# Optimization experiments

Hardware: AMD Instinct MI355X
Metric: run time of the kernel (lower is better)

## Reference

```python
import math
import jax, jax.numpy as jnp
import numpy as np

NUM_HEADS = 16

def _alibi_slopes(n):
    def pow2(n):
        start = 2 ** (-2 ** (-(math.log2(n) - 3)))
        return [start * start ** i for i in range(n)]
    if math.log2(n).is_integer():
        return pow2(n)
    c = 2 ** math.floor(math.log2(n))
    return pow2(c) + _alibi_slopes(2 * c)[0::2][: n - c]

def _alibi_bias(num_heads, L):
    pos = np.arange(L)
    rel = (pos[None, :] - pos[:, None]).astype(np.float32)  # [L, L]
    slopes = np.asarray(_alibi_slopes(num_heads), dtype=np.float32)[:, None, None]
    bias = slopes * rel[None, :, :]  # [H, L, L]
    causal = pos[None, :] <= pos[:, None]
    bias = np.where(causal[None, :, :], bias, -np.inf).astype(np.float32)
    return jnp.asarray(bias)[None]  # [1, H, L, L]

def setup_inputs() -> dict:
    key = jax.random.key(0)
    ks = jax.random.split(key, 4)
    B, L, D = 2, 2048, 1024
    x = jax.random.normal(ks[0], (B, L, D), dtype=jnp.float32)
    W_in = jax.random.normal(ks[1], (D, 3 * D), dtype=jnp.float32) * 0.02
    b_in = jnp.zeros((3 * D,), dtype=jnp.float32)
    W_out = jax.random.normal(ks[2], (D, D), dtype=jnp.float32) * 0.02
    b_out = jnp.zeros((D,), dtype=jnp.float32)
    return {"x": x, "W_in": W_in, "b_in": b_in, "W_out": W_out, "b_out": b_out}

def reference(x, W_in, b_in, W_out, b_out):
    B, L, D = x.shape
    H = NUM_HEADS
    Dh = D // H
    qkv = x @ W_in + b_in  # [B, L, 3D]
    q, k, v = jnp.split(qkv, 3, axis=-1)
    # [B, H, L, Dh]
    q = q.reshape(B, L, H, Dh).transpose(0, 2, 1, 3)
    k = k.reshape(B, L, H, Dh).transpose(0, 2, 1, 3)
    v = v.reshape(B, L, H, Dh).transpose(0, 2, 1, 3)
    attn = jnp.einsum("bhqd,bhkd->bhqk", q, k) * (1.0 / math.sqrt(Dh))
    attn = attn + _alibi_bias(H, L)  # ALiBi + causal mask (-inf above diag)
    p = jax.nn.softmax(attn, axis=-1)
    out = jnp.einsum("bhqk,bhkd->bhqd", p, v)
    out = out.transpose(0, 2, 1, 3).reshape(B, L, D)
    out = out @ W_out + b_out
    return out, k, v
```

## Files before the change

### kernel.cpp

```cpp
#include <hip/hip_runtime.h>
#include <math.h>

typedef __bf16 bf16x8 __attribute__((ext_vector_type(8)));
typedef float  f32x4  __attribute__((ext_vector_type(4)));
typedef unsigned short u16x4 __attribute__((ext_vector_type(4)));

#define BATCH  2
#define SEQ    2048
#define DMODEL 1024
#define NHEAD  16
#define DHEAD  64
#define MROWS  4096
#define N_QKV  3072
#define KDIM   1024
#define OUTSECT (MROWS*DMODEL)

#define LOG2E 1.44269504088896f
#define QSCALE (0.125f * LOG2E)

__device__ inline __bf16 f2bf(float f) {
    unsigned u = __builtin_bit_cast(unsigned, f);
    unsigned r = (u + 0x7fffu + ((u >> 16) & 1u)) >> 16;
    return __builtin_bit_cast(__bf16, (unsigned short)r);
}

__device__ inline void gload16(const void* g, void* l) {
    __builtin_amdgcn_global_load_lds(
        (const __attribute__((address_space(1))) void*)g,
        (__attribute__((address_space(3))) void*)l, 16, 0, 0);
}

__device__ inline float dpp_max16(float x) {
    int v, t;
    v = __builtin_bit_cast(int, x);
    t = __builtin_amdgcn_update_dpp(v, v, 0xB1, 0xF, 0xF, false);
    x = fmaxf(x, __builtin_bit_cast(float, t));
    v = __builtin_bit_cast(int, x);
    t = __builtin_amdgcn_update_dpp(v, v, 0x4E, 0xF, 0xF, false);
    x = fmaxf(x, __builtin_bit_cast(float, t));
    v = __builtin_bit_cast(int, x);
    t = __builtin_amdgcn_update_dpp(v, v, 0x128, 0xF, 0xF, false);
    x = fmaxf(x, __builtin_bit_cast(float, t));
    v = __builtin_bit_cast(int, x);
    t = __builtin_amdgcn_update_dpp(v, v, 0x140, 0xF, 0xF, false);
    x = fmaxf(x, __builtin_bit_cast(float, t));
    return x;
}
__device__ inline float dpp_sum16(float x) {
    int v, t;
    v = __builtin_bit_cast(int, x);
    t = __builtin_amdgcn_update_dpp(v, v, 0xB1, 0xF, 0xF, false);
    x += __builtin_bit_cast(float, t);
    v = __builtin_bit_cast(int, x);
    t = __builtin_amdgcn_update_dpp(v, v, 0x4E, 0xF, 0xF, false);
    x += __builtin_bit_cast(float, t);
    v = __builtin_bit_cast(int, x);
    t = __builtin_amdgcn_update_dpp(v, v, 0x128, 0xF, 0xF, false);
    x += __builtin_bit_cast(float, t);
    v = __builtin_bit_cast(int, x);
    t = __builtin_amdgcn_update_dpp(v, v, 0x140, 0xF, 0xF, false);
    x += __builtin_bit_cast(float, t);
    return x;
}

__global__ __launch_bounds__(256) void cvt_all_k(
    const float* __restrict__ x, __bf16* __restrict__ xb,
    const float* __restrict__ W_in, __bf16* __restrict__ wti,
    const float* __restrict__ W_out, __bf16* __restrict__ wto)
{
    __shared__ float t[64][65];
    const int b = blockIdx.x;
    const int tid = threadIdx.x;
    if (b < 2048) {
        size_t i = (size_t)b * 256 + tid;
        const float4* p = (const float4*)x + i * 2;
        float4 a = p[0], c = p[1];
        __bf16 o[8] = {f2bf(a.x), f2bf(a.y), f2bf(a.z), f2bf(a.w),
                       f2bf(c.x), f2bf(c.y), f2bf(c.z), f2bf(c.w)};
        *(bf16x8*)(xb + i * 8) = *(bf16x8*)o;
        return;
    }
    const float* W;  __bf16* Wt;  int Nw, bx, by;
    if (b < 2816) { int c = b - 2048; W = W_in;  Wt = wti; Nw = N_QKV;  bx = c % 48; by = c / 48; }
    else          { int c = b - 2816; W = W_out; Wt = wto; Nw = DMODEL; bx = c % 16; by = c / 16; }
    const int k0 = by * 64, n0 = bx * 64;
    #pragma unroll
    for (int u = 0; u < 4; ++u) {
        int idx = u * 256 + tid;
        int r = idx >> 4, c4 = (idx & 15) << 2;
        float4 v = *(const float4*)&W[(size_t)(k0 + r) * Nw + n0 + c4];
        t[r][c4] = v.x; t[r][c4 + 1] = v.y; t[r][c4 + 2] = v.z; t[r][c4 + 3] = v.w;
    }
    __syncthreads();
    #pragma unroll
    for (int u = 0; u < 2; ++u) {
        int idx = u * 256 + tid;
        int n = idx >> 3, k8 = (idx & 7) << 3;
        __bf16 o[8];
        #pragma unroll
        for (int i = 0; i < 8; ++i) o[i] = f2bf(t[k8 + i][n]);
        *(bf16x8*)&Wt[(size_t)(n0 + n) * KDIM + k0 + k8] = *(bf16x8*)o;
    }
}

template<int MODE, int FI, int FJ>
__global__ __launch_bounds__(256) void gemm_bf(
    const __bf16* __restrict__ A, const __bf16* __restrict__ Bt,
    const float* __restrict__ bias,
    float* __restrict__ fo, float* __restrict__ kf, float* __restrict__ vf,
    __bf16* __restrict__ qb, __bf16* __restrict__ kb, __bf16* __restrict__ vb,
    int nbx)
{
    constexpr int BMt = FI * 32, BNt = FJ * 32;
    __shared__ __align__(16) __bf16 As[BMt * 64];
    __shared__ __align__(16) __bf16 Bs[BNt * 64];

    const int tid = threadIdx.x, wid = tid >> 6, lane = tid & 63;
    const int l16 = lane & 15, lq = lane >> 4;
    const int wm = wid >> 1, wn = wid & 1;

    const int nwg = gridDim.x;
    const int bid = blockIdx.x;
    const int swz = (bid & 7) * (nwg >> 3) + (bid >> 3);
    const int m0 = (swz / nbx) * BMt;
    const int n0 = (swz % nbx) * BNt;

    const int lr8 = lane >> 3;
    const int colE = ((lane & 7) ^ lr8) << 3;

    f32x4 acc[FI][FJ];
    #pragma unroll
    for (int i = 0; i < FI; ++i)
        #pragma unroll
        for (int j = 0; j < FJ; ++j)
            acc[i][j] = f32x4{0.f, 0.f, 0.f, 0.f};

    for (int k0 = 0; k0 < KDIM; k0 += 64) {
        __syncthreads();
        #pragma unroll
        for (int c = wid; c < FI * 4 + FJ * 4; c += 4) {
            const bool isA = (c < FI * 4);
            const int ch = isA ? c : c - FI * 4;
            const int row = ch * 8 + lr8;
            const __bf16* src = isA ? (A  + (size_t)(m0 + row) * KDIM + k0 + colE)
                                    : (Bt + (size_t)(n0 + row) * KDIM + k0 + colE);
            gload16(src, (isA ? As : Bs) + ch * 512);
        }
        __syncthreads();
        #pragma unroll
        for (int kk = 0; kk < 2; ++kk) {
            bf16x8 af[FI], bfg[FJ];
            #pragma unroll
            for (int i = 0; i < FI; ++i) {
                int r = wm * (FI * 16) + i * 16 + l16;
                af[i] = *(const bf16x8*)&As[r * 64 + ((kk * 32 + lq * 8) ^ ((r & 7) << 3))];
            }
            #pragma unroll
            for (int j = 0; j < FJ; ++j) {
                int r = wn * (FJ * 16) + j * 16 + l16;
                bfg[j] = *(const bf16x8*)&Bs[r * 64 + ((kk * 32 + lq * 8) ^ ((r & 7) << 3))];
            }
            #pragma unroll
            for (int i = 0; i < FI; ++i)
                #pragma unroll
                for (int j = 0; j < FJ; ++j)
                    acc[i][j] = __builtin_amdgcn_mfma_f32_16x16x32_bf16(af[i], bfg[j], acc[i][j], 0, 0, 0);
        }
    }

    #pragma unroll
    for (int i = 0; i < FI; ++i) {
        #pragma unroll
        for (int j = 0; j < FJ; ++j) {
            const int col  = n0 + wn * (FJ * 16) + j * 16 + l16;
            const int rowb = m0 + wm * (FI * 16) + i * 16 + lq * 4;
            float v[4];
            #pragma unroll
            for (int r = 0; r < 4; ++r) v[r] = acc[i][j][r] + bias[col];
            if (MODE == 1) {
                #pragma unroll
                for (int r = 0; r < 4; ++r)
                    fo[(size_t)(rowb + r) * DMODEL + col] = v[r];
            } else {
                const int which = col >> 10, rem = col & 1023;
                const int h = rem >> 6, dh = rem & 63;
                const int bb = rowb >> 11, ll = rowb & 2047;
                const size_t lidx = ((size_t)(bb * NHEAD + h) * SEQ + ll) * DHEAD + dh;
                if (which == 0) {
                    #pragma unroll
                    for (int r = 0; r < 4; ++r)
                        qb[lidx + (size_t)r * DHEAD] = f2bf(v[r] * QSCALE);
                } else if (which == 1) {
                    #pragma unroll
                    for (int r = 0; r < 4; ++r) {
                        kf[lidx + (size_t)r * DHEAD] = v[r];
                        kb[lidx + (size_t)r * DHEAD] = f2bf(v[r]);
                    }
                } else {
                    u16x4 pk;
                    #pragma unroll
                    for (int r = 0; r < 4; ++r) {
                        vf[lidx + (size_t)r * DHEAD] = v[r];
                        pk[r] = __builtin_bit_cast(unsigned short, f2bf(v[r]));
                    }
                    *(u16x4*)&vb[((size_t)(bb * NHEAD + h) * DHEAD + dh) * SEQ + ll] = pk;
                }
            }
        }
    }
}

__global__ __launch_bounds__(256) void attn_k(
    const __bf16* __restrict__ Qb, const __bf16* __restrict__ Kb,
    const __bf16* __restrict__ Vb, __bf16* __restrict__ Ob)
{
    __shared__ __align__(16) __bf16 QP[4096];
    __shared__ __align__(16) __bf16 Ks[2][64 * 64];
    __shared__ __align__(16) __bf16 Vs[2][64 * 64];

    const int tid = threadIdx.x, wid = tid >> 6, lane = tid & 63;
    const int l16 = lane & 15, lq = lane >> 4;

    const int bid = blockIdx.x;
    const int xcd = bid & 7, t = bid >> 3;
    const int p = t >> 5, s = t & 31, a = s >> 2;
    const int qt = (p == 0) ? (31 - a) : (p == 1) ? (16 + a)
                 : (p == 2) ? (15 - a) : a;
    const int bh = xcd * 4 + (s & 3);
    const int h = bh & 15, bb = bh >> 4;
    const int q0 = qt * 64;
    const size_t kvbase = (size_t)bh * SEQ * DHEAD;
    const float slope2 = exp2f(-0.5f * (float)(h + 1)) * LOG2E;
    const int qr0 = wid * 16;
    const int lr8 = lane >> 3;
    const int colE = ((lane & 7) ^ lr8) << 3;

    #pragma unroll
    for (int u = 0; u < 2; ++u) {
        int ch = u * 4 + wid;
        int row = ch * 8 + lr8;
        gload16(Qb + kvbase + (size_t)(q0 + row) * DHEAD + colE, QP + ch * 512);
    }
    #pragma unroll
    for (int u = 0; u < 2; ++u) {
        int ch = u * 4 + wid;
        int row = ch * 8 + lr8;
        gload16(Kb + kvbase + (size_t)row * DHEAD + colE, Ks[0] + ch * 512);
        gload16(Vb + kvbase + (size_t)row * SEQ  + colE, Vs[0] + ch * 512);
    }
    __syncthreads();

    const int qrow = qr0 + l16;
    const bf16x8 aq0 = *(const bf16x8*)&QP[qrow * 64 + ((lq * 8) ^ ((qrow & 7) << 3))];
    const bf16x8 aq1 = *(const bf16x8*)&QP[qrow * 64 + ((32 + lq * 8) ^ ((qrow & 7) << 3))];

    float ct[4][4];
    #pragma unroll
    for (int r = 0; r < 4; ++r) {
        const int qi = q0 + qr0 + lq * 4 + r;
        #pragma unroll
        for (int nf = 0; nf < 4; ++nf)
            ct[r][nf] = slope2 * (float)(nf * 16 + l16 - qi);
    }
    const float dtj = slope2 * 64.f;

    float mrow[4], lrow[4];
    f32x4 accO[4];
    #pragma unroll
    for (int r = 0; r < 4; ++r) { mrow[r] = -1e30f; lrow[r] = 0.f; }
    #pragma unroll
    for (int j = 0; j < 4; ++j) accO[j] = f32x4{0.f, 0.f, 0.f, 0.f};

    int cur = 0;
    for (int jt = 0; jt <= qt; ++jt) {
        if (jt < qt) {
            const int jn = (jt + 1) * 64;
            #pragma unroll
            for (int u = 0; u < 2; ++u) {
                int ch = u * 4 + wid;
                int row = ch * 8 + lr8;
                gload16(Kb + kvbase + (size_t)(jn + row) * DHEAD + colE, Ks[cur ^ 1] + ch * 512);
                gload16(Vb + kvbase + (size_t)row * SEQ + jn + colE,     Vs[cur ^ 1] + ch * 512);
            }
        }

        const float tb = dtj * (float)jt;
        f32x4 s[4];
        #pragma unroll
        for (int nf = 0; nf < 4; ++nf) {
            #pragma unroll
            for (int r = 0; r < 4; ++r) s[nf][r] = ct[r][nf] + tb;
        }
        if (jt == qt) {
            #pragma unroll
            for (int nf = 0; nf < 4; ++nf)
                #pragma unroll
                for (int r = 0; r < 4; ++r)
                    if (nf * 16 + l16 > qr0 + lq * 4 + r) s[nf][r] = -3e38f;
        }

        __builtin_amdgcn_s_setprio(1);
        #pragma unroll
        for (int nf = 0; nf < 4; ++nf) {
            int kr = nf * 16 + l16;
            bf16x8 bk0 = *(const bf16x8*)&Ks[cur][kr * 64 + ((lq * 8) ^ ((kr & 7) << 3))];
            bf16x8 bk1 = *(const bf16x8*)&Ks[cur][kr * 64 + ((32 + lq * 8) ^ ((kr & 7) << 3))];
            s[nf] = __builtin_amdgcn_mfma_f32_16x16x32_bf16(aq0, bk0, s[nf], 0, 0, 0);
            s[nf] = __builtin_amdgcn_mfma_f32_16x16x32_bf16(aq1, bk1, s[nf], 0, 0, 0);
        }
        __builtin_amdgcn_s_setprio(0);

        float rm[4];
        #pragma unroll
        for (int r = 0; r < 4; ++r)
            rm[r] = dpp_max16(fmaxf(fmaxf(s[0][r], s[1][r]), fmaxf(s[2][r], s[3][r])));
        bool need = (rm[0] > mrow[0] + 8.f) || (rm[1] > mrow[1] + 8.f) ||
                    (rm[2] > mrow[2] + 8.f) || (rm[3] > mrow[3] + 8.f);
        if (__any(need)) {
            #pragma unroll
            for (int r = 0; r < 4; ++r) {
                float mnew = fmaxf(mrow[r], rm[r]);
                float scale = __builtin_amdgcn_exp2f(mrow[r] - mnew);
                lrow[r] *= scale;
                mrow[r] = mnew;
                #pragma unroll
                for (int nf = 0; nf < 4; ++nf) accO[nf][r] *= scale;
            }
        }
        #pragma unroll
        for (int r = 0; r < 4; ++r) {
            float p0 = __builtin_amdgcn_exp2f(s[0][r] - mrow[r]);
            float p1 = __builtin_amdgcn_exp2f(s[1][r] - mrow[r]);
            float p2 = __builtin_amdgcn_exp2f(s[2][r] - mrow[r]);
            float p3 = __builtin_amdgcn_exp2f(s[3][r] - mrow[r]);
            const int prow = lq * 4 + r;
            const int pb = wid * 1024 + prow * 64;
            const int px = (prow & 7) << 3;
            QP[pb + ((l16     ) ^ px)] = (__bf16)p0;
            QP[pb + ((l16 + 16) ^ px)] = (__bf16)p1;
            QP[pb + ((l16 + 32) ^ px)] = (__bf16)p2;
            QP[pb + ((l16 + 48) ^ px)] = (__bf16)p3;
            lrow[r] += dpp_sum16((p0 + p1) + (p2 + p3));
        }

        bf16x8 ap0 = *(const bf16x8*)&QP[wid * 1024 + l16 * 64 + ((lq * 8) ^ ((l16 & 7) << 3))];
        bf16x8 ap1 = *(const bf16x8*)&QP[wid * 1024 + l16 * 64 + ((32 + lq * 8) ^ ((l16 & 7) << 3))];
        __builtin_amdgcn_s_setprio(1);
        #pragma unroll
        for (int nf = 0; nf < 4; ++nf) {
            int vr = nf * 16 + l16;
            bf16x8 bv0 = *(const bf16x8*)&Vs[cur][vr * 64 + ((lq * 8) ^ ((vr & 7) << 3))];
            bf16x8 bv1 = *(const bf16x8*)&Vs[cur][vr * 64 + ((32 + lq * 8) ^ ((vr & 7) << 3))];
            accO[nf] = __builtin_amdgcn_mfma_f32_16x16x32_bf16(ap0, bv0, accO[nf], 0, 0, 0);
            accO[nf] = __builtin_amdgcn_mfma_f32_16x16x32_bf16(ap1, bv1, accO[nf], 0, 0, 0);
        }
        __builtin_amdgcn_s_setprio(0);

        __syncthreads();
        cur ^= 1;
    }

    #pragma unroll
    for (int r = 0; r < 4; ++r) {
        const float inv = __builtin_amdgcn_rcpf(lrow[r]);
        const int qi = q0 + qr0 + lq * 4 + r;
        #pragma unroll
        for (int nf = 0; nf < 4; ++nf) {
            int dh = nf * 16 + l16;
            Ob[(size_t)(bb * SEQ + qi) * DMODEL + h * DHEAD + dh] = (__bf16)(accO[nf][r] * inv);
        }
    }
}

extern "C" void kernel_launch(void* const* d_in, const int* in_sizes, int n_in,
                              void* d_out, int out_size, void* d_ws, size_t ws_size,
                              hipStream_t stream) {
    const float* x     = (const float*)d_in[0];
    const float* W_in  = (const float*)d_in[1];
    const float* b_in  = (const float*)d_in[2];
    const float* W_out = (const float*)d_in[3];
    const float* b_out = (const float*)d_in[4];

    float* out = (float*)d_out;
    float* kf  = out + (size_t)OUTSECT;
    float* vf  = out + 2 * (size_t)OUTSECT;

    __bf16* qb = (__bf16*)d_out;
    __bf16* xb = (__bf16*)d_out + (size_t)OUTSECT;

    __bf16* ob  = (__bf16*)d_ws;
    __bf16* kb  = ob + (size_t)OUTSECT;
    __bf16* vb  = kb + (size_t)OUTSECT;
    __bf16* wti = vb + (size_t)OUTSECT;
    __bf16* wto = wti + (size_t)N_QKV * KDIM;

    cvt_all_k<<<3072, 256, 0, stream>>>(x, xb, W_in, wti, W_out, wto);

    gemm_bf<0, 4, 4><<<768, 256, 0, stream>>>(xb, wti, b_in,
        nullptr, kf, vf, qb, kb, vb, N_QKV / 128);

    attn_k<<<1024, 256, 0, stream>>>(qb, kb, vb, ob);

    gemm_bf<1, 4, 4><<<256, 256, 0, stream>>>(ob, wto, b_out,
        out, nullptr, nullptr, nullptr, nullptr, nullptr, DMODEL / 128);
}
```

Baseline: 202.3 us.

## Widen attention query tile to 128 rows per block, halving K/V reloads

```diff
diff --git a/kernel.cpp b/kernel.cpp
--- a/kernel.cpp
+++ b/kernel.cpp
@@ -214,7 +214,7 @@
     const __bf16* __restrict__ Qb, const __bf16* __restrict__ Kb,
     const __bf16* __restrict__ Vb, __bf16* __restrict__ Ob)
 {
-    __shared__ __align__(16) __bf16 QP[4096];
+    __shared__ __align__(16) __bf16 QP[128 * 64];
     __shared__ __align__(16) __bf16 Ks[2][64 * 64];
     __shared__ __align__(16) __bf16 Vs[2][64 * 64];
 
@@ -224,19 +224,18 @@
     const int bid = blockIdx.x;
     const int xcd = bid & 7, t = bid >> 3;
     const int p = t >> 5, s = t & 31, a = s >> 2;
-    const int qt = (p == 0) ? (31 - a) : (p == 1) ? (16 + a)
-                 : (p == 2) ? (15 - a) : a;
+    const int qc = p ? a : (15 - a);
     const int bh = xcd * 4 + (s & 3);
     const int h = bh & 15, bb = bh >> 4;
-    const int q0 = qt * 64;
+    const int q0 = qc * 128;
+    const int jtop = 2 * qc + 1;
     const size_t kvbase = (size_t)bh * SEQ * DHEAD;
     const float slope2 = exp2f(-0.5f * (float)(h + 1)) * LOG2E;
-    const int qr0 = wid * 16;
     const int lr8 = lane >> 3;
     const int colE = ((lane & 7) ^ lr8) << 3;
 
     #pragma unroll
-    for (int u = 0; u < 2; ++u) {
+    for (int u = 0; u < 4; ++u) {
         int ch = u * 4 + wid;
         int row = ch * 8 + lr8;
         gload16(Qb + kvbase + (size_t)(q0 + row) * DHEAD + colE, QP + ch * 512);
@@ -250,31 +249,41 @@
     }
     __syncthreads();
 
-    const int qrow = qr0 + l16;
-    const bf16x8 aq0 = *(const bf16x8*)&QP[qrow * 64 + ((lq * 8) ^ ((qrow & 7) << 3))];
-    const bf16x8 aq1 = *(const bf16x8*)&QP[qrow * 64 + ((32 + lq * 8) ^ ((qrow & 7) << 3))];
-
-    float ct[4][4];
+    bf16x8 aq[2][2];
+    #pragma unroll
+    for (int mi = 0; mi < 2; ++mi) {
+        const int qrow = wid * 32 + mi * 16 + l16;
+        aq[mi][0] = *(const bf16x8*)&QP[qrow * 64 + ((lq * 8) ^ ((qrow & 7) << 3))];
+        aq[mi][1] = *(const bf16x8*)&QP[qrow * 64 + ((32 + lq * 8) ^ ((qrow & 7) << 3))];
+    }
+
+    float ct0[4][4];
     #pragma unroll
     for (int r = 0; r < 4; ++r) {
-        const int qi = q0 + qr0 + lq * 4 + r;
+        const int qi0 = q0 + wid * 32 + lq * 4 + r;
         #pragma unroll
         for (int nf = 0; nf < 4; ++nf)
-            ct[r][nf] = slope2 * (float)(nf * 16 + l16 - qi);
+            ct0[r][nf] = slope2 * (float)(nf * 16 + l16 - qi0);
     }
     const float dtj = slope2 * 64.f;
-
-    float mrow[4], lrow[4];
-    f32x4 accO[4];
-    #pragma unroll
-    for (int r = 0; r < 4; ++r) { mrow[r] = -1e30f; lrow[r] = 0.f; }
-    #pragma unroll
-    for (int j = 0; j < 4; ++j) accO[j] = f32x4{0.f, 0.f, 0.f, 0.f};
+    const float d16 = slope2 * 16.f;
+
+    float mrow[2][4], lrow[2][4];
+    f32x4 accO[2][4];
+    #pragma unroll
+    for (int mi = 0; mi < 2; ++mi)
+        #pragma unroll
+        for (int r = 0; r < 4; ++r) {
+            mrow[mi][r] = -1e30f; lrow[mi][r] = 0.f;
+            accO[mi][r] = f32x4{0.f, 0.f, 0.f, 0.f};
+        }
 
     int cur = 0;
-    for (int jt = 0; jt <= qt; ++jt) {
-        if (jt < qt) {
-            const int jn = (jt + 1) * 64;
+    for (int jt = 0; jt <= jtop; ++jt) {
+        const int j0 = jt * 64;
+
+        if (jt < jtop) {
+            const int jn = j0 + 64;
             #pragma unroll
             for (int u = 0; u < 2; ++u) {
                 int ch = u * 4 + wid;
@@ -284,90 +293,126 @@
             }
         }
 
+        const int relB = q0 + wid * 32 - j0;
         const float tb = dtj * (float)jt;
-        f32x4 s[4];
-        #pragma unroll
-        for (int nf = 0; nf < 4; ++nf) {
-            #pragma unroll
-            for (int r = 0; r < 4; ++r) s[nf][r] = ct[r][nf] + tb;
-        }
-        if (jt == qt) {
-            #pragma unroll
-            for (int nf = 0; nf < 4; ++nf)
-                #pragma unroll
-                for (int r = 0; r < 4; ++r)
-                    if (nf * 16 + l16 > qr0 + lq * 4 + r) s[nf][r] = -3e38f;
-        }
-
-        __builtin_amdgcn_s_setprio(1);
-        #pragma unroll
-        for (int nf = 0; nf < 4; ++nf) {
-            int kr = nf * 16 + l16;
-            bf16x8 bk0 = *(const bf16x8*)&Ks[cur][kr * 64 + ((lq * 8) ^ ((kr & 7) << 3))];
-            bf16x8 bk1 = *(const bf16x8*)&Ks[cur][kr * 64 + ((32 + lq * 8) ^ ((kr & 7) << 3))];
-            s[nf] = __builtin_amdgcn_mfma_f32_16x16x32_bf16(aq0, bk0, s[nf], 0, 0, 0);
-            s[nf] = __builtin_amdgcn_mfma_f32_16x16x32_bf16(aq1, bk1, s[nf], 0, 0, 0);
-        }
-        __builtin_amdgcn_s_setprio(0);
-
-        float rm[4];
-        #pragma unroll
-        for (int r = 0; r < 4; ++r)
-            rm[r] = dpp_max16(fmaxf(fmaxf(s[0][r], s[1][r]), fmaxf(s[2][r], s[3][r])));
-        bool need = (rm[0] > mrow[0] + 8.f) || (rm[1] > mrow[1] + 8.f) ||
-                    (rm[2] > mrow[2] + 8.f) || (rm[3] > mrow[3] + 8.f);
+        f32x4 sf[2][4];
+        float inm[2][4];
+
+        #pragma unroll
+        for (int mi = 0; mi < 2; ++mi) {
+            const int rel = relB + mi * 16;
+            if (rel > -16) {
+                const float bias = tb - d16 * (float)mi;
+                #pragma unroll
+                for (int nf = 0; nf < 4; ++nf)
+                    #pragma unroll
+                    for (int r = 0; r < 4; ++r) sf[mi][nf][r] = ct0[r][nf] + bias;
+                if (rel < 64) {
+                    #pragma unroll
+                    for (int nf = 0; nf < 4; ++nf)
+                        #pragma unroll
+                        for (int r = 0; r < 4; ++r)
+                            if (nf * 16 + l16 > rel + lq * 4 + r) sf[mi][nf][r] = -3e38f;
+                }
+                __builtin_amdgcn_s_setprio(1);
+                #pragma unroll
+                for (int nf = 0; nf < 4; ++nf) {
+                    int kr = nf * 16 + l16;
+                    bf16x8 bk0 = *(const bf16x8*)&Ks[cur][kr * 64 + ((lq * 8) ^ ((kr & 7) << 3))];
+                    bf16x8 bk1 = *(const bf16x8*)&Ks[cur][kr * 64 + ((32 + lq * 8) ^ ((kr & 7) << 3))];
+                    sf[mi][nf] = __builtin_amdgcn_mfma_f32_16x16x32_bf16(aq[mi][0], bk0, sf[mi][nf], 0, 0, 0);
+                    sf[mi][nf] = __builtin_amdgcn_mfma_f32_16x16x32_bf16(aq[mi][1], bk1, sf[mi][nf], 0, 0, 0);
+                }
+                __builtin_amdgcn_s_setprio(0);
+            }
+        }
+
+        bool need = false;
+        #pragma unroll
+        for (int mi = 0; mi < 2; ++mi) {
+            if (relB + mi * 16 > -16) {
+                #pragma unroll
+                for (int r = 0; r < 4; ++r) {
+                    inm[mi][r] = fmaxf(fmaxf(sf[mi][0][r], sf[mi][1][r]),
+                                       fmaxf(sf[mi][2][r], sf[mi][3][r]));
+                    need = need || (inm[mi][r] > mrow[mi][r] + 8.f);
+                }
+            }
+        }
         if (__any(need)) {
             #pragma unroll
-            for (int r = 0; r < 4; ++r) {
-                float mnew = fmaxf(mrow[r], rm[r]);
-                float scale = __builtin_amdgcn_exp2f(mrow[r] - mnew);
-                lrow[r] *= scale;
-                mrow[r] = mnew;
-                #pragma unroll
-                for (int nf = 0; nf < 4; ++nf) accO[nf][r] *= scale;
-            }
-        }
-        #pragma unroll
-        for (int r = 0; r < 4; ++r) {
-            float p0 = __builtin_amdgcn_exp2f(s[0][r] - mrow[r]);
-            float p1 = __builtin_amdgcn_exp2f(s[1][r] - mrow[r]);
-            float p2 = __builtin_amdgcn_exp2f(s[2][r] - mrow[r]);
-            float p3 = __builtin_amdgcn_exp2f(s[3][r] - mrow[r]);
-            const int prow = lq * 4 + r;
-            const int pb = wid * 1024 + prow * 64;
-            const int px = (prow & 7) << 3;
-            QP[pb + ((l16     ) ^ px)] = (__bf16)p0;
-            QP[pb + ((l16 + 16) ^ px)] = (__bf16)p1;
-            QP[pb + ((l16 + 32) ^ px)] = (__bf16)p2;
-            QP[pb + ((l16 + 48) ^ px)] = (__bf16)p3;
-            lrow[r] += dpp_sum16((p0 + p1) + (p2 + p3));
-        }
-
-        bf16x8 ap0 = *(const bf16x8*)&QP[wid * 1024 + l16 * 64 + ((lq * 8) ^ ((l16 & 7) << 3))];
-        bf16x8 ap1 = *(const bf16x8*)&QP[wid * 1024 + l16 * 64 + ((32 + lq * 8) ^ ((l16 & 7) << 3))];
-        __builtin_amdgcn_s_setprio(1);
-        #pragma unroll
-        for (int nf = 0; nf < 4; ++nf) {
-            int vr = nf * 16 + l16;
-            bf16x8 bv0 = *(const bf16x8*)&Vs[cur][vr * 64 + ((lq * 8) ^ ((vr & 7) << 3))];
-            bf16x8 bv1 = *(const bf16x8*)&Vs[cur][vr * 64 + ((32 + lq * 8) ^ ((vr & 7) << 3))];
-            accO[nf] = __builtin_amdgcn_mfma_f32_16x16x32_bf16(ap0, bv0, accO[nf], 0, 0, 0);
-            accO[nf] = __builtin_amdgcn_mfma_f32_16x16x32_bf16(ap1, bv1, accO[nf], 0, 0, 0);
-        }
-        __builtin_amdgcn_s_setprio(0);
+            for (int mi = 0; mi < 2; ++mi) {
+                if (relB + mi * 16 > -16) {
+                    #pragma unroll
+                    for (int r = 0; r < 4; ++r) {
+                        float rm = dpp_max16(inm[mi][r]);
+                        float mnew = fmaxf(mrow[mi][r], rm);
+                        float scale = __builtin_amdgcn_exp2f(mrow[mi][r] - mnew);
+                        lrow[mi][r] *= scale;
+                        mrow[mi][r] = mnew;
+                        #pragma unroll
+                        for (int nf = 0; nf < 4; ++nf) accO[mi][nf][r] *= scale;
+                    }
+                }
+            }
+        }
+
+        #pragma unroll
+        for (int mi = 0; mi < 2; ++mi) {
+            if (relB + mi * 16 > -16) {
+                #pragma unroll
+                for (int r = 0; r < 4; ++r) {
+                    float p0 = __builtin_amdgcn_exp2f(sf[mi][0][r] - mrow[mi][r]);
+                    float p1 = __builtin_amdgcn_exp2f(sf[mi][1][r] - mrow[mi][r]);
+                    float p2 = __builtin_amdgcn_exp2f(sf[mi][2][r] - mrow[mi][r]);
+                    float p3 = __builtin_amdgcn_exp2f(sf[mi][3][r] - mrow[mi][r]);
+                    const int prow = wid * 32 + mi * 16 + lq * 4 + r;
+                    const int pb = prow * 64;
+                    const int px = (prow & 7) << 3;
+                    QP[pb + ((l16     ) ^ px)] = (__bf16)p0;
+                    QP[pb + ((l16 + 16) ^ px)] = (__bf16)p1;
+                    QP[pb + ((l16 + 32) ^ px)] = (__bf16)p2;
+                    QP[pb + ((l16 + 48) ^ px)] = (__bf16)p3;
+                    lrow[mi][r] += (p0 + p1) + (p2 + p3);
+                }
+            }
+        }
+
+        #pragma unroll
+        for (int mi = 0; mi < 2; ++mi) {
+            if (relB + mi * 16 > -16) {
+                const int arow = wid * 32 + mi * 16 + l16;
+                bf16x8 ap0 = *(const bf16x8*)&QP[arow * 64 + ((lq * 8) ^ ((arow & 7) << 3))];
+                bf16x8 ap1 = *(const bf16x8*)&QP[arow * 64 + ((32 + lq * 8) ^ ((arow & 7) << 3))];
+                __builtin_amdgcn_s_setprio(1);
+                #pragma unroll
+                for (int nf = 0; nf < 4; ++nf) {
+                    int vr = nf * 16 + l16;
+                    bf16x8 bv0 = *(const bf16x8*)&Vs[cur][vr * 64 + ((lq * 8) ^ ((vr & 7) << 3))];
+                    bf16x8 bv1 = *(const bf16x8*)&Vs[cur][vr * 64 + ((32 + lq * 8) ^ ((vr & 7) << 3))];
+                    accO[mi][nf] = __builtin_amdgcn_mfma_f32_16x16x32_bf16(ap0, bv0, accO[mi][nf], 0, 0, 0);
+                    accO[mi][nf] = __builtin_amdgcn_mfma_f32_16x16x32_bf16(ap1, bv1, accO[mi][nf], 0, 0, 0);
+                }
+                __builtin_amdgcn_s_setprio(0);
+            }
+        }
 
         __syncthreads();
         cur ^= 1;
     }
 
     #pragma unroll
-    for (int r = 0; r < 4; ++r) {
-        const float inv = __builtin_amdgcn_rcpf(lrow[r]);
-        const int qi = q0 + qr0 + lq * 4 + r;
-        #pragma unroll
-        for (int nf = 0; nf < 4; ++nf) {
-            int dh = nf * 16 + l16;
-            Ob[(size_t)(bb * SEQ + qi) * DMODEL + h * DHEAD + dh] = (__bf16)(accO[nf][r] * inv);
+    for (int mi = 0; mi < 2; ++mi) {
+        #pragma unroll
+        for (int r = 0; r < 4; ++r) {
+            const float ltot = dpp_sum16(lrow[mi][r]);
+            const float inv = __builtin_amdgcn_rcpf(ltot);
+            const int qi = q0 + wid * 32 + mi * 16 + lq * 4 + r;
+            #pragma unroll
+            for (int nf = 0; nf < 4; ++nf) {
+                int dh = nf * 16 + l16;
+                Ob[(size_t)(bb * SEQ + qi) * DMODEL + h * DHEAD + dh] = (__bf16)(accO[mi][nf][r] * inv);
+            }
         }
     }
 }
@@ -399,7 +444,7 @@
     gemm_bf<0, 4, 4><<<768, 256, 0, stream>>>(xb, wti, b_in,
         nullptr, kf, vf, qb, kb, vb, N_QKV / 128);
 
-    attn_k<<<1024, 256, 0, stream>>>(qb, kb, vb, ob);
+    attn_k<<<512, 256, 0, stream>>>(qb, kb, vb, ob);
 
     gemm_bf<1, 4, 4><<<256, 256, 0, stream>>>(ob, wto, b_out,
         out, nullptr, nullptr, nullptr, nullptr, nullptr, DMODEL / 128);
```

Result: slower. 222.4 us (+9.9%).

## Double-buffer GEMM shared-memory tiles with BK=32 to overlap loads and MFMA

Applied to the files above, without the earlier changes.

```diff
diff --git a/kernel.cpp b/kernel.cpp
--- a/kernel.cpp
+++ b/kernel.cpp
@@ -103,7 +103,7 @@
     }
 }
 
-template<int MODE, int FI, int FJ>
+template<int MODE>
 __global__ __launch_bounds__(256) void gemm_bf(
     const __bf16* __restrict__ A, const __bf16* __restrict__ Bt,
     const float* __restrict__ bias,
@@ -111,9 +111,8 @@
     __bf16* __restrict__ qb, __bf16* __restrict__ kb, __bf16* __restrict__ vb,
     int nbx)
 {
-    constexpr int BMt = FI * 32, BNt = FJ * 32;
-    __shared__ __align__(16) __bf16 As[BMt * 64];
-    __shared__ __align__(16) __bf16 Bs[BNt * 64];
+    __shared__ __align__(16) __bf16 As[2][128 * 32];
+    __shared__ __align__(16) __bf16 Bs[2][128 * 32];
 
     const int tid = threadIdx.x, wid = tid >> 6, lane = tid & 63;
     const int l16 = lane & 15, lq = lane >> 4;
@@ -122,58 +121,67 @@
     const int nwg = gridDim.x;
     const int bid = blockIdx.x;
     const int swz = (bid & 7) * (nwg >> 3) + (bid >> 3);
-    const int m0 = (swz / nbx) * BMt;
-    const int n0 = (swz % nbx) * BNt;
-
-    const int lr8 = lane >> 3;
-    const int colE = ((lane & 7) ^ lr8) << 3;
-
-    f32x4 acc[FI][FJ];
-    #pragma unroll
-    for (int i = 0; i < FI; ++i)
-        #pragma unroll
-        for (int j = 0; j < FJ; ++j)
+    const int m0 = (swz / nbx) * 128;
+    const int n0 = (swz % nbx) * 128;
+
+    const int lr4  = lane >> 2;
+    const int gcol = (((lane & 3) ^ (lr4 & 3)) << 3);
+
+    f32x4 acc[4][4];
+    #pragma unroll
+    for (int i = 0; i < 4; ++i)
+        #pragma unroll
+        for (int j = 0; j < 4; ++j)
             acc[i][j] = f32x4{0.f, 0.f, 0.f, 0.f};
 
-    for (int k0 = 0; k0 < KDIM; k0 += 64) {
+#define GSTAGE(buf, kk0) do {                                                   \
+    _Pragma("unroll")                                                           \
+    for (int u = 0; u < 4; ++u) {                                               \
+        const int c = u * 4 + wid;                                              \
+        const bool isA = (c < 8);                                               \
+        const int ch = isA ? c : c - 8;                                         \
+        const __bf16* src = isA                                                 \
+            ? (A  + (size_t)(m0 + ch * 16 + lr4) * KDIM + (kk0) + gcol)         \
+            : (Bt + (size_t)(n0 + ch * 16 + lr4) * KDIM + (kk0) + gcol);        \
+        gload16(src, (isA ? As[buf] : Bs[buf]) + ch * 512);                     \
+    }                                                                           \
+} while (0)
+
+    GSTAGE(0, 0);
+    __syncthreads();
+
+    int cur = 0;
+    for (int ks = 0; ks < KDIM / 32; ++ks) {
+        if (ks < KDIM / 32 - 1) GSTAGE(cur ^ 1, (ks + 1) * 32);
+
+        bf16x8 af[4], bfg[4];
+        #pragma unroll
+        for (int i = 0; i < 4; ++i) {
+            const int r = wm * 64 + i * 16 + l16;
+            af[i] = *(const bf16x8*)&As[cur][r * 32 + ((lq ^ (r & 3)) << 3)];
+        }
+        #pragma unroll
+        for (int j = 0; j < 4; ++j) {
+            const int r = wn * 64 + j * 16 + l16;
+            bfg[j] = *(const bf16x8*)&Bs[cur][r * 32 + ((lq ^ (r & 3)) << 3)];
+        }
+        #pragma unroll
+        for (int i = 0; i < 4; ++i)
+            #pragma unroll
+            for (int j = 0; j < 4; ++j)
+                acc[i][j] = __builtin_amdgcn_mfma_f32_16x16x32_bf16(af[i], bfg[j], acc[i][j], 0, 0, 0);
+
         __syncthreads();
-        #pragma unroll
-        for (int c = wid; c < FI * 4 + FJ * 4; c += 4) {
-            const bool isA = (c < FI * 4);
-            const int ch = isA ? c : c - FI * 4;
-            const int row = ch * 8 + lr8;
-            const __bf16* src = isA ? (A  + (size_t)(m0 + row) * KDIM + k0 + colE)
-                                    : (Bt + (size_t)(n0 + row) * KDIM + k0 + colE);
-            gload16(src, (isA ? As : Bs) + ch * 512);
-        }
-        __syncthreads();
-        #pragma unroll
-        for (int kk = 0; kk < 2; ++kk) {
-            bf16x8 af[FI], bfg[FJ];
-            #pragma unroll
-            for (int i = 0; i < FI; ++i) {
-                int r = wm * (FI * 16) + i * 16 + l16;
-                af[i] = *(const bf16x8*)&As[r * 64 + ((kk * 32 + lq * 8) ^ ((r & 7) << 3))];
-            }
-            #pragma unroll
-            for (int j = 0; j < FJ; ++j) {
-                int r = wn * (FJ * 16) + j * 16 + l16;
-                bfg[j] = *(const bf16x8*)&Bs[r * 64 + ((kk * 32 + lq * 8) ^ ((r & 7) << 3))];
-            }
-            #pragma unroll
-            for (int i = 0; i < FI; ++i)
-                #pragma unroll
-                for (int j = 0; j < FJ; ++j)
-                    acc[i][j] = __builtin_amdgcn_mfma_f32_16x16x32_bf16(af[i], bfg[j], acc[i][j], 0, 0, 0);
-        }
-    }
-
-    #pragma unroll
-    for (int i = 0; i < FI; ++i) {
-        #pragma unroll
-        for (int j = 0; j < FJ; ++j) {
-            const int col  = n0 + wn * (FJ * 16) + j * 16 + l16;
-            const int rowb = m0 + wm * (FI * 16) + i * 16 + lq * 4;
+        cur ^= 1;
+    }
+#undef GSTAGE
+
+    #pragma unroll
+    for (int i = 0; i < 4; ++i) {
+        #pragma unroll
+        for (int j = 0; j < 4; ++j) {
+            const int col  = n0 + wn * 64 + j * 16 + l16;
+            const int rowb = m0 + wm * 64 + i * 16 + lq * 4;
             float v[4];
             #pragma unroll
             for (int r = 0; r < 4; ++r) v[r] = acc[i][j][r] + bias[col];
@@ -285,18 +293,18 @@
         }
 
         const float tb = dtj * (float)jt;
-        f32x4 s[4];
+        f32x4 sv[4];
         #pragma unroll
         for (int nf = 0; nf < 4; ++nf) {
             #pragma unroll
-            for (int r = 0; r < 4; ++r) s[nf][r] = ct[r][nf] + tb;
+            for (int r = 0; r < 4; ++r) sv[nf][r] = ct[r][nf] + tb;
         }
         if (jt == qt) {
             #pragma unroll
             for (int nf = 0; nf < 4; ++nf)
                 #pragma unroll
                 for (int r = 0; r < 4; ++r)
-                    if (nf * 16 + l16 > qr0 + lq * 4 + r) s[nf][r] = -3e38f;
+                    if (nf * 16 + l16 > qr0 + lq * 4 + r) sv[nf][r] = -3e38f;
         }
 
         __builtin_amdgcn_s_setprio(1);
@@ -305,15 +313,15 @@
             int kr = nf * 16 + l16;
             bf16x8 bk0 = *(const bf16x8*)&Ks[cur][kr * 64 + ((lq * 8) ^ ((kr & 7) << 3))];
             bf16x8 bk1 = *(const bf16x8*)&Ks[cur][kr * 64 + ((32 + lq * 8) ^ ((kr & 7) << 3))];
-            s[nf] = __builtin_amdgcn_mfma_f32_16x16x32_bf16(aq0, bk0, s[nf], 0, 0, 0);
-            s[nf] = __builtin_amdgcn_mfma_f32_16x16x32_bf16(aq1, bk1, s[nf], 0, 0, 0);
+            sv[nf] = __builtin_amdgcn_mfma_f32_16x16x32_bf16(aq0, bk0, sv[nf], 0, 0, 0);
+            sv[nf] = __builtin_amdgcn_mfma_f32_16x16x32_bf16(aq1, bk1, sv[nf], 0, 0, 0);
         }
         __builtin_amdgcn_s_setprio(0);
 
         float rm[4];
         #pragma unroll
         for (int r = 0; r < 4; ++r)
-            rm[r] = dpp_max16(fmaxf(fmaxf(s[0][r], s[1][r]), fmaxf(s[2][r], s[3][r])));
+            rm[r] = dpp_max16(fmaxf(fmaxf(sv[0][r], sv[1][r]), fmaxf(sv[2][r], sv[3][r])));
         bool need = (rm[0] > mrow[0] + 8.f) || (rm[1] > mrow[1] + 8.f) ||
                     (rm[2] > mrow[2] + 8.f) || (rm[3] > mrow[3] + 8.f);
         if (__any(need)) {
@@ -329,10 +337,10 @@
         }
         #pragma unroll
         for (int r = 0; r < 4; ++r) {
-            float p0 = __builtin_amdgcn_exp2f(s[0][r] - mrow[r]);
-            float p1 = __builtin_amdgcn_exp2f(s[1][r] - mrow[r]);
-            float p2 = __builtin_amdgcn_exp2f(s[2][r] - mrow[r]);
-            float p3 = __builtin_amdgcn_exp2f(s[3][r] - mrow[r]);
+            float p0 = __builtin_amdgcn_exp2f(sv[0][r] - mrow[r]);
+            float p1 = __builtin_amdgcn_exp2f(sv[1][r] - mrow[r]);
+            float p2 = __builtin_amdgcn_exp2f(sv[2][r] - mrow[r]);
+            float p3 = __builtin_amdgcn_exp2f(sv[3][r] - mrow[r]);
             const int prow = lq * 4 + r;
             const int pb = wid * 1024 + prow * 64;
             const int px = (prow & 7) << 3;
@@ -396,11 +404,11 @@
 
     cvt_all_k<<<3072, 256, 0, stream>>>(x, xb, W_in, wti, W_out, wto);
 
-    gemm_bf<0, 4, 4><<<768, 256, 0, stream>>>(xb, wti, b_in,
+    gemm_bf<0><<<768, 256, 0, stream>>>(xb, wti, b_in,
         nullptr, kf, vf, qb, kb, vb, N_QKV / 128);
 
     attn_k<<<1024, 256, 0, stream>>>(qb, kb, vb, ob);
 
-    gemm_bf<1, 4, 4><<<256, 256, 0, stream>>>(ob, wto, b_out,
+    gemm_bf<1><<<256, 256, 0, stream>>>(ob, wto, b_out,
         out, nullptr, nullptr, nullptr, nullptr, nullptr, DMODEL / 128);
 }
```

After: 214.2 us. 1.06x slower.
